# Kernel optimization log

Measured on AMD Instinct MI355X. Metric: run time of the kernel, lower is better.

## Reference

```python
import jax, jax.numpy as jnp
import numpy as np

D_MODEL = 1024
NHEAD = 16
HEAD_DIM = D_MODEL // NHEAD
B, S = 4, 2048


def setup_inputs() -> dict:
    key = jax.random.key(0)
    ks = jax.random.split(key, 10)
    scale = 1.0 / np.sqrt(D_MODEL)
    inp = {
        "x": jax.random.normal(ks[0], (B, S, D_MODEL), dtype=jnp.float32),
        "y": jax.random.normal(ks[1], (B, S, D_MODEL), dtype=jnp.float32),
        "wq": jax.random.normal(ks[2], (D_MODEL, D_MODEL), dtype=jnp.float32) * scale,
        "bq": jnp.zeros((D_MODEL,), dtype=jnp.float32),
        "wk": jax.random.normal(ks[3], (D_MODEL, D_MODEL), dtype=jnp.float32) * scale,
        "bk": jnp.zeros((D_MODEL,), dtype=jnp.float32),
        "wv": jax.random.normal(ks[4], (D_MODEL, D_MODEL), dtype=jnp.float32) * scale,
        "bv": jnp.zeros((D_MODEL,), dtype=jnp.float32),
        "wo": jax.random.normal(ks[5], (D_MODEL, D_MODEL), dtype=jnp.float32) * scale,
        "bo": jnp.zeros((D_MODEL,), dtype=jnp.float32),
    }
    return inp


def reference(x, y, wq, bq, wk, bk, wv, bv, wo, bo):
    # Linear projections (torch nn.Linear: x @ W.T + b; here weights stored as [in, out])
    q = x @ wq + bq  # [B, S, D]
    k = y @ wk + bk
    v = y @ wv + bv
    # split heads -> [B, H, S, Dh]
    def heads(t):
        return t.reshape(B, S, NHEAD, HEAD_DIM).transpose(0, 2, 1, 3)
    q, k, v = heads(q), heads(k), heads(v)
    scores = jnp.einsum("bhqd,bhkd->bhqk", q, k) / jnp.sqrt(jnp.float32(HEAD_DIM))
    attn = jax.nn.softmax(scores, axis=-1)  # dropout = identity in eval mode
    out = jnp.einsum("bhqk,bhkd->bhqd", attn, v)
    out = out.transpose(0, 2, 1, 3).reshape(B, S, D_MODEL)
    return out @ wo + bo
```

## Files before the change

### kernel.cpp

```cpp
#include <hip/hip_runtime.h>
#include <stdint.h>

#define D_MODEL 1024
#define NHEAD 16
#define HEAD_DIM 64
#define BATCH 4
#define SEQ 2048
#define ROWS (BATCH*SEQ)

typedef __attribute__((ext_vector_type(8))) short short8;
typedef __attribute__((ext_vector_type(4))) float f32x4;
typedef __attribute__((ext_vector_type(2))) unsigned int u32x2;
typedef unsigned short u16;
typedef unsigned int u32;

#define QSCALE 0.18033688011112042f

__device__ __forceinline__ u16 f2b(float f) {
  union { float f; uint32_t u; } in; in.f = f;
  uint32_t u = in.u;
  return (u16)((u + 0x7FFFu + ((u >> 16) & 1u)) >> 16);
}

__device__ __forceinline__ void async_lds16(const void* g, void* l) {
  __builtin_amdgcn_global_load_lds(
      (const __attribute__((address_space(1))) uint32_t*)g,
      (__attribute__((address_space(3))) uint32_t*)l,
      16, 0, 0);
}

__device__ __forceinline__ u32 pack_bf16(float lo, float hi) {
  union { float f; uint32_t u; } a, b; a.f = lo; b.f = hi;
  return __builtin_amdgcn_perm(b.u + 0x8000u, a.u + 0x8000u, 0x07060302u);
}

__global__ void __launch_bounds__(256) cvt_kernel(const float* __restrict__ in,
                                                  u16* __restrict__ out) {
  int i = blockIdx.x * 256 + threadIdx.x;
  float4 v = ((const float4*)in)[i];
  ushort4 o;
  o.x = f2b(v.x); o.y = f2b(v.y); o.z = f2b(v.z); o.w = f2b(v.w);
  ((ushort4*)out)[i] = o;
}

__global__ void __launch_bounds__(256) wtrans_kernel(const float* __restrict__ w,
                                                     u16* __restrict__ wt) {
  __shared__ u16 tile[64 * 65];
  int t = threadIdx.x;
  int c = t & 63, rb = t >> 6;
  int k0 = blockIdx.x * 64, n0 = blockIdx.y * 64;
#pragma unroll
  for (int i = 0; i < 16; ++i) {
    int r = rb + i * 4;
    tile[c * 65 + r] = f2b(w[(size_t)(k0 + r) * D_MODEL + n0 + c]);
  }
  __syncthreads();
#pragma unroll
  for (int i = 0; i < 16; ++i) {
    int r = rb + i * 4;
    wt[(size_t)(n0 + r) * D_MODEL + k0 + c] = tile[r * 65 + c];
  }
}

template <int MODE>
__device__ __forceinline__ void gemm_bt_core(const u16* __restrict__ A,
                                             const u16* __restrict__ Bt,
                                             const float* __restrict__ bias,
                                             void* __restrict__ Cout, float scale) {
  constexpr int K = 1024, N = 1024;
  __shared__ u16 As[128 * 32];
  __shared__ u16 Bs[128 * 32];
  int tid = threadIdx.x;
  int wave = tid >> 6, lane = tid & 63;
  int quad = lane >> 4, l16 = lane & 15;
  int wm = wave & 1, wn = wave >> 1;
  int m0 = blockIdx.y * 128, n0 = blockIdx.x * 128;

  f32x4 acc[4][4];
#pragma unroll
  for (int mi = 0; mi < 4; ++mi)
#pragma unroll
    for (int ni = 0; ni < 4; ++ni) acc[mi][ni] = f32x4{0.f, 0.f, 0.f, 0.f};

  int srow = lane >> 2;
  int scol = (lane & 3) * 16;

  for (int k0 = 0; k0 < K; k0 += 32) {
#pragma unroll
    for (int i = 0; i < 2; ++i) {
      int c = wave * 2 + i;
      const char* ga = (const char*)(A + (size_t)(m0 + c * 16 + srow) * K + k0) + scol;
      async_lds16(ga, (char*)As + c * 1024);
      const char* gb = (const char*)(Bt + (size_t)(n0 + c * 16 + srow) * K + k0) + scol;
      async_lds16(gb, (char*)Bs + c * 1024);
    }
    __syncthreads();

    short8 af[4], bf[4];
#pragma unroll
    for (int mi = 0; mi < 4; ++mi)
      af[mi] = *(const short8*)(As + (wm * 64 + mi * 16 + l16) * 32 + quad * 8);
#pragma unroll
    for (int ni = 0; ni < 4; ++ni)
      bf[ni] = *(const short8*)(Bs + (wn * 64 + ni * 16 + l16) * 32 + quad * 8);
#pragma unroll
    for (int mi = 0; mi < 4; ++mi)
#pragma unroll
      for (int ni = 0; ni < 4; ++ni)
        acc[mi][ni] = __builtin_amdgcn_mfma_f32_16x16x32_bf16(af[mi], bf[ni], acc[mi][ni], 0, 0, 0);
    __syncthreads();
  }

  if (MODE == 2) {
#pragma unroll
    for (int ni = 0; ni < 4; ++ni) {
      int col = n0 + wn * 64 + ni * 16 + l16;
      int bb = col >> 11, ss = col & 2047;
      size_t sbase = (size_t)(ss & ~63) + 4 * l16 + ni;
#pragma unroll
      for (int mi = 0; mi < 4; ++mi) {
        int row0 = m0 + wm * 64 + mi * 16 + quad * 4;
#pragma unroll
        for (int r = 0; r < 4; ++r) {
          int dcol = row0 + r;
          float vv = acc[mi][ni][r] + bias[dcol];
          int hh = dcol >> 6, dd = dcol & 63;
          size_t vtrow = ((size_t)bb * 16 + hh) * 64 + dd;
          ((u16*)Cout)[vtrow * 2048 + sbase] = f2b(vv);
        }
      }
    }
  } else {
#pragma unroll
    for (int ni = 0; ni < 4; ++ni) {
      int col = n0 + wn * 64 + ni * 16 + l16;
      float bv = bias[col];
#pragma unroll
      for (int mi = 0; mi < 4; ++mi) {
        int row = m0 + wm * 64 + mi * 16 + quad * 4;
#pragma unroll
        for (int r = 0; r < 4; ++r) {
          float vv = (acc[mi][ni][r] + bv) * scale;
          if (MODE == 1)
            ((float*)Cout)[(size_t)(row + r) * N + col] = vv;
          else
            ((u16*)Cout)[(size_t)(row + r) * N + col] = f2b(vv);
        }
      }
    }
  }
}

__global__ void __launch_bounds__(256) gemm_qk_kernel(
    const u16* __restrict__ xb, const u16* __restrict__ yb,
    const u16* __restrict__ wqT, const u16* __restrict__ wkT,
    const float* __restrict__ bq, const float* __restrict__ bk,
    u16* __restrict__ q, u16* __restrict__ k) {
  if (blockIdx.z == 0)
    gemm_bt_core<0>(xb, wqT, bq, q, QSCALE);
  else
    gemm_bt_core<0>(yb, wkT, bk, k, 1.0f);
}

__global__ void __launch_bounds__(256) gemm_v_kernel(const u16* __restrict__ wvT,
                                                     const u16* __restrict__ yb,
                                                     const float* __restrict__ bv,
                                                     u16* __restrict__ vt) {
  gemm_bt_core<2>(wvT, yb, bv, vt, 1.0f);
}

__global__ void __launch_bounds__(256) gemm_o_kernel(const u16* __restrict__ ao,
                                                     const u16* __restrict__ woT,
                                                     const float* __restrict__ bo,
                                                     float* __restrict__ out) {
  gemm_bt_core<1>(ao, woT, bo, out, 1.0f);
}

__global__ void __launch_bounds__(256, 4) attn_kernel(const u16* __restrict__ Q,
                                                      const u16* __restrict__ Kp,
                                                      const u16* __restrict__ Vt,
                                                      u16* __restrict__ Outp) {
  __shared__ u16 Ks[64 * 64];
  __shared__ u16 Vts[64 * 64];
  __shared__ u16 Ps[4][32 * 64];

  int tid = threadIdx.x, wave = tid >> 6, lane = tid & 63;
  int quad = lane >> 4, l16 = lane & 15;
  int bh = blockIdx.y;
  int b = bh >> 4, h = bh & 15;
  int q0 = blockIdx.x * 128 + wave * 32;
  size_t gbase = (size_t)b * SEQ * D_MODEL;
  const u16* kbase = Kp + gbase + (size_t)h * HEAD_DIM;
  const u16* vbase = Vt + (size_t)bh * HEAD_DIM * SEQ;
  const u16* qrow = Q + gbase + (size_t)q0 * D_MODEL + (size_t)h * HEAD_DIM;

  short8 aq[2][2];
#pragma unroll
  for (int rs = 0; rs < 2; ++rs)
#pragma unroll
    for (int dc = 0; dc < 2; ++dc)
      aq[rs][dc] = *(const short8*)(qrow + (size_t)(rs * 16 + l16) * D_MODEL + dc * 32 + quad * 8);

  f32x4 Oacc[2][4];
  float lpart[2][4];
#pragma unroll
  for (int rs = 0; rs < 2; ++rs)
#pragma unroll
    for (int ni = 0; ni < 4; ++ni) Oacc[rs][ni] = f32x4{0.f, 0.f, 0.f, 0.f};
#pragma unroll
  for (int rs = 0; rs < 2; ++rs)
#pragma unroll
    for (int r = 0; r < 4; ++r) lpart[rs][r] = 0.f;

  size_t koff[2], voff[2];
  int dstoff[2];
#pragma unroll
  for (int i = 0; i < 2; ++i) {
    int c = i * 256 + tid;
    int krow = c >> 3, kgp = c & 7;
    koff[i] = (size_t)krow * D_MODEL + (size_t)((kgp ^ (krow & 7)) * 8);
    voff[i] = (size_t)krow * SEQ + (size_t)((kgp ^ (krow & 7)) * 8);
    dstoff[i] = i * 4096 + wave * 1024;
  }

  for (int kv0 = 0; kv0 < SEQ; kv0 += 64) {
    __syncthreads();
#pragma unroll
    for (int i = 0; i < 2; ++i) {
      async_lds16(kbase + (size_t)kv0 * D_MODEL + koff[i], (char*)Ks + dstoff[i]);
      async_lds16(vbase + (size_t)kv0 + voff[i], (char*)Vts + dstoff[i]);
    }
    __syncthreads();

    u16* Pw = Ps[wave];
#pragma unroll
    for (int rs = 0; rs < 2; ++rs) {
      f32x4 S[4];
#pragma unroll
      for (int sub = 0; sub < 4; ++sub) {
        int key = sub * 16 + l16;
        int x = l16 & 7;
        short8 b0 = *(const short8*)(Ks + key * 64 + ((quad ^ x) << 3));
        short8 b1 = *(const short8*)(Ks + key * 64 + (((4 + quad) ^ x) << 3));
        f32x4 s = f32x4{0.f, 0.f, 0.f, 0.f};
        s = __builtin_amdgcn_mfma_f32_16x16x32_bf16(aq[rs][0], b0, s, 0, 0, 0);
        s = __builtin_amdgcn_mfma_f32_16x16x32_bf16(aq[rs][1], b1, s, 0, 0, 0);
        S[sub] = s;
      }
#pragma unroll
      for (int r = 0; r < 4; ++r) {
        float p0 = __builtin_amdgcn_exp2f(S[0][r]);
        float p1 = __builtin_amdgcn_exp2f(S[1][r]);
        float p2 = __builtin_amdgcn_exp2f(S[2][r]);
        float p3 = __builtin_amdgcn_exp2f(S[3][r]);
        lpart[rs][r] += (p0 + p1) + (p2 + p3);
        u32 lo = pack_bf16(p0, p1);
        u32 hi = pack_bf16(p2, p3);
        int row = rs * 16 + quad * 4 + r;
        int off = row * 64 + (((l16 >> 1) ^ (row & 7)) << 3) + ((l16 & 1) << 2);
        *(u32x2*)(Pw + off) = u32x2{lo, hi};
      }
    }

#pragma unroll
    for (int kc = 0; kc < 2; ++kc) {
      short8 pa[2];
#pragma unroll
      for (int rs = 0; rs < 2; ++rs) {
        int prow = rs * 16 + l16;
        pa[rs] = *(const short8*)(Pw + prow * 64 + ((((kc << 2) + quad) ^ (l16 & 7)) << 3));
      }
#pragma unroll
      for (int ni = 0; ni < 4; ++ni) {
        int d = ni * 16 + l16;
        short8 bv = *(const short8*)(Vts + d * 64 + ((((kc << 2) + quad) ^ (l16 & 7)) << 3));
        Oacc[0][ni] = __builtin_amdgcn_mfma_f32_16x16x32_bf16(pa[0], bv, Oacc[0][ni], 0, 0, 0);
        Oacc[1][ni] = __builtin_amdgcn_mfma_f32_16x16x32_bf16(pa[1], bv, Oacc[1][ni], 0, 0, 0);
      }
    }
  }

#pragma unroll
  for (int rs = 0; rs < 2; ++rs)
#pragma unroll
    for (int r = 0; r < 4; ++r) {
      float l = lpart[rs][r];
      l += __shfl_xor(l, 1);
      l += __shfl_xor(l, 2);
      l += __shfl_xor(l, 4);
      l += __shfl_xor(l, 8);
      float inv = 1.0f / l;
      size_t orow = gbase + (size_t)(q0 + rs * 16 + quad * 4 + r) * D_MODEL + (size_t)h * HEAD_DIM;
#pragma unroll
      for (int ni = 0; ni < 4; ++ni)
        Outp[orow + ni * 16 + l16] = f2b(Oacc[rs][ni][r] * inv);
    }
}

extern "C" void kernel_launch(void* const* d_in, const int* in_sizes, int n_in,
                              void* d_out, int out_size, void* d_ws, size_t ws_size,
                              hipStream_t stream) {
  const float* x  = (const float*)d_in[0];
  const float* y  = (const float*)d_in[1];
  const float* wq = (const float*)d_in[2];
  const float* bq = (const float*)d_in[3];
  const float* wk = (const float*)d_in[4];
  const float* bk = (const float*)d_in[5];
  const float* wv = (const float*)d_in[6];
  const float* bv = (const float*)d_in[7];
  const float* wo = (const float*)d_in[8];
  const float* bo = (const float*)d_in[9];
  float* out = (float*)d_out;

  char* ws = (char*)d_ws;
  const size_t SZ_ACT = (size_t)ROWS * D_MODEL * 2;
  const size_t SZ_W   = (size_t)D_MODEL * D_MODEL * 2;
  u16* xb  = (u16*)(ws);
  u16* yb  = (u16*)(ws + SZ_ACT);
  u16* wqT = (u16*)(ws + 2 * SZ_ACT);
  u16* wkT = (u16*)(ws + 2 * SZ_ACT + SZ_W);
  u16* wvT = (u16*)(ws + 2 * SZ_ACT + 2 * SZ_W);
  u16* woT = (u16*)(ws + 2 * SZ_ACT + 3 * SZ_W);
  u16* qb  = (u16*)(ws + 2 * SZ_ACT + 4 * SZ_W);
  u16* kb  = (u16*)(ws + 3 * SZ_ACT + 4 * SZ_W);
  u16* vt  = (u16*)(ws + 4 * SZ_ACT + 4 * SZ_W);
  u16* ao  = (u16*)(ws + 5 * SZ_ACT + 4 * SZ_W);

  cvt_kernel<<<8192, 256, 0, stream>>>(x, xb);
  cvt_kernel<<<8192, 256, 0, stream>>>(y, yb);
  wtrans_kernel<<<dim3(16, 16), 256, 0, stream>>>(wq, wqT);
  wtrans_kernel<<<dim3(16, 16), 256, 0, stream>>>(wk, wkT);
  wtrans_kernel<<<dim3(16, 16), 256, 0, stream>>>(wv, wvT);
  wtrans_kernel<<<dim3(16, 16), 256, 0, stream>>>(wo, woT);
  gemm_qk_kernel<<<dim3(8, 64, 2), 256, 0, stream>>>(xb, yb, wqT, wkT, bq, bk, qb, kb);
  gemm_v_kernel<<<dim3(64, 8), 256, 0, stream>>>(wvT, yb, bv, vt);
  attn_kernel<<<dim3(16, 64), 256, 0, stream>>>(qb, kb, vt, ao);
  gemm_o_kernel<<<dim3(8, 64), 256, 0, stream>>>(ao, woT, bo, out);
}
```

Baseline: 346.3 us.

## Double-buffer attention K/V tiles, merge launches, and reorder attention grid

```diff
diff --git a/kernel.cpp b/kernel.cpp
--- a/kernel.cpp
+++ b/kernel.cpp
@@ -34,8 +34,12 @@
   return __builtin_amdgcn_perm(b.u + 0x8000u, a.u + 0x8000u, 0x07060302u);
 }
 
-__global__ void __launch_bounds__(256) cvt_kernel(const float* __restrict__ in,
-                                                  u16* __restrict__ out) {
+__global__ void __launch_bounds__(256) cvt_kernel(const float* __restrict__ x,
+                                                  const float* __restrict__ y,
+                                                  u16* __restrict__ xb,
+                                                  u16* __restrict__ yb) {
+  const float* in = blockIdx.y ? y : x;
+  u16* out = blockIdx.y ? yb : xb;
   int i = blockIdx.x * 256 + threadIdx.x;
   float4 v = ((const float4*)in)[i];
   ushort4 o;
@@ -43,9 +47,15 @@
   ((ushort4*)out)[i] = o;
 }
 
-__global__ void __launch_bounds__(256) wtrans_kernel(const float* __restrict__ w,
-                                                     u16* __restrict__ wt) {
+__global__ void __launch_bounds__(256) wtrans_kernel(const float* __restrict__ wq,
+                                                     const float* __restrict__ wk,
+                                                     const float* __restrict__ wv,
+                                                     const float* __restrict__ wo,
+                                                     u16* __restrict__ wtbase) {
   __shared__ u16 tile[64 * 65];
+  int z = blockIdx.z;
+  const float* w = (z == 0) ? wq : (z == 1 ? wk : (z == 2 ? wv : wo));
+  u16* wt = wtbase + (size_t)z * D_MODEL * D_MODEL;
   int t = threadIdx.x;
   int c = t & 63, rb = t >> 6;
   int k0 = blockIdx.x * 64, n0 = blockIdx.y * 64;
@@ -66,7 +76,8 @@
 __device__ __forceinline__ void gemm_bt_core(const u16* __restrict__ A,
                                              const u16* __restrict__ Bt,
                                              const float* __restrict__ bias,
-                                             void* __restrict__ Cout, float scale) {
+                                             void* __restrict__ Cout, float scale,
+                                             int m0, int n0) {
   constexpr int K = 1024, N = 1024;
   __shared__ u16 As[128 * 32];
   __shared__ u16 Bs[128 * 32];
@@ -74,7 +85,6 @@
   int wave = tid >> 6, lane = tid & 63;
   int quad = lane >> 4, l16 = lane & 15;
   int wm = wave & 1, wn = wave >> 1;
-  int m0 = blockIdx.y * 128, n0 = blockIdx.x * 128;
 
   f32x4 acc[4][4];
 #pragma unroll
@@ -151,44 +161,41 @@
   }
 }
 
-__global__ void __launch_bounds__(256) gemm_qk_kernel(
+__global__ void __launch_bounds__(256) gemm_qkv_kernel(
     const u16* __restrict__ xb, const u16* __restrict__ yb,
-    const u16* __restrict__ wqT, const u16* __restrict__ wkT,
-    const float* __restrict__ bq, const float* __restrict__ bk,
-    u16* __restrict__ q, u16* __restrict__ k) {
-  if (blockIdx.z == 0)
-    gemm_bt_core<0>(xb, wqT, bq, q, QSCALE);
-  else
-    gemm_bt_core<0>(yb, wkT, bk, k, 1.0f);
-}
-
-__global__ void __launch_bounds__(256) gemm_v_kernel(const u16* __restrict__ wvT,
-                                                     const u16* __restrict__ yb,
-                                                     const float* __restrict__ bv,
-                                                     u16* __restrict__ vt) {
-  gemm_bt_core<2>(wvT, yb, bv, vt, 1.0f);
+    const u16* __restrict__ wqT, const u16* __restrict__ wkT, const u16* __restrict__ wvT,
+    const float* __restrict__ bq, const float* __restrict__ bk, const float* __restrict__ bv,
+    u16* __restrict__ q, u16* __restrict__ k, u16* __restrict__ vt) {
+  int bx = blockIdx.x, z = blockIdx.y;
+  if (z == 0) {
+    gemm_bt_core<0>(xb, wqT, bq, q, QSCALE, (bx >> 3) * 128, (bx & 7) * 128);
+  } else if (z == 1) {
+    gemm_bt_core<0>(yb, wkT, bk, k, 1.0f, (bx >> 3) * 128, (bx & 7) * 128);
+  } else {
+    gemm_bt_core<2>(wvT, yb, bv, vt, 1.0f, (bx & 7) * 128, (bx >> 3) * 128);
+  }
 }
 
 __global__ void __launch_bounds__(256) gemm_o_kernel(const u16* __restrict__ ao,
                                                      const u16* __restrict__ woT,
                                                      const float* __restrict__ bo,
                                                      float* __restrict__ out) {
-  gemm_bt_core<1>(ao, woT, bo, out, 1.0f);
+  gemm_bt_core<1>(ao, woT, bo, out, 1.0f, blockIdx.y * 128, blockIdx.x * 128);
 }
 
 __global__ void __launch_bounds__(256, 4) attn_kernel(const u16* __restrict__ Q,
                                                       const u16* __restrict__ Kp,
                                                       const u16* __restrict__ Vt,
                                                       u16* __restrict__ Outp) {
-  __shared__ u16 Ks[64 * 64];
-  __shared__ u16 Vts[64 * 64];
+  __shared__ u16 Ks[2][64 * 64];
+  __shared__ u16 Vts[2][64 * 64];
   __shared__ u16 Ps[4][32 * 64];
 
   int tid = threadIdx.x, wave = tid >> 6, lane = tid & 63;
   int quad = lane >> 4, l16 = lane & 15;
-  int bh = blockIdx.y;
+  int bh = blockIdx.x;
   int b = bh >> 4, h = bh & 15;
-  int q0 = blockIdx.x * 128 + wave * 32;
+  int q0 = blockIdx.y * 128 + wave * 32;
   size_t gbase = (size_t)b * SEQ * D_MODEL;
   const u16* kbase = Kp + gbase + (size_t)h * HEAD_DIM;
   const u16* vbase = Vt + (size_t)bh * HEAD_DIM * SEQ;
@@ -223,28 +230,46 @@
     dstoff[i] = i * 4096 + wave * 1024;
   }
 
-  for (int kv0 = 0; kv0 < SEQ; kv0 += 64) {
+#pragma unroll
+  for (int i = 0; i < 2; ++i) {
+    async_lds16(kbase + koff[i], (char*)Ks[0] + dstoff[i]);
+    async_lds16(vbase + voff[i], (char*)Vts[0] + dstoff[i]);
+  }
+
+  constexpr int NT = SEQ / 64;
+  for (int t = 0; t < NT; ++t) {
+    int cur = t & 1;
     __syncthreads();
-#pragma unroll
-    for (int i = 0; i < 2; ++i) {
-      async_lds16(kbase + (size_t)kv0 * D_MODEL + koff[i], (char*)Ks + dstoff[i]);
-      async_lds16(vbase + (size_t)kv0 + voff[i], (char*)Vts + dstoff[i]);
-    }
-    __syncthreads();
-
+    if (t + 1 < NT) {
+      size_t kvoff = (size_t)(t + 1) * 64;
+#pragma unroll
+      for (int i = 0; i < 2; ++i) {
+        async_lds16(kbase + kvoff * D_MODEL + koff[i], (char*)Ks[cur ^ 1] + dstoff[i]);
+        async_lds16(vbase + kvoff + voff[i], (char*)Vts[cur ^ 1] + dstoff[i]);
+      }
+    }
+
+    const u16* Kc = Ks[cur];
+    const u16* Vc = Vts[cur];
     u16* Pw = Ps[wave];
+    int x = l16 & 7;
+
+    short8 kf[4][2];
+#pragma unroll
+    for (int sub = 0; sub < 4; ++sub) {
+      const u16* kr = Kc + (sub * 16 + l16) * 64;
+      kf[sub][0] = *(const short8*)(kr + ((quad ^ x) << 3));
+      kf[sub][1] = *(const short8*)(kr + (((4 + quad) ^ x) << 3));
+    }
+
 #pragma unroll
     for (int rs = 0; rs < 2; ++rs) {
       f32x4 S[4];
 #pragma unroll
       for (int sub = 0; sub < 4; ++sub) {
-        int key = sub * 16 + l16;
-        int x = l16 & 7;
-        short8 b0 = *(const short8*)(Ks + key * 64 + ((quad ^ x) << 3));
-        short8 b1 = *(const short8*)(Ks + key * 64 + (((4 + quad) ^ x) << 3));
         f32x4 s = f32x4{0.f, 0.f, 0.f, 0.f};
-        s = __builtin_amdgcn_mfma_f32_16x16x32_bf16(aq[rs][0], b0, s, 0, 0, 0);
-        s = __builtin_amdgcn_mfma_f32_16x16x32_bf16(aq[rs][1], b1, s, 0, 0, 0);
+        s = __builtin_amdgcn_mfma_f32_16x16x32_bf16(aq[rs][0], kf[sub][0], s, 0, 0, 0);
+        s = __builtin_amdgcn_mfma_f32_16x16x32_bf16(aq[rs][1], kf[sub][1], s, 0, 0, 0);
         S[sub] = s;
       }
 #pragma unroll
@@ -268,12 +293,12 @@
 #pragma unroll
       for (int rs = 0; rs < 2; ++rs) {
         int prow = rs * 16 + l16;
-        pa[rs] = *(const short8*)(Pw + prow * 64 + ((((kc << 2) + quad) ^ (l16 & 7)) << 3));
+        pa[rs] = *(const short8*)(Pw + prow * 64 + ((((kc << 2) + quad) ^ x) << 3));
       }
 #pragma unroll
       for (int ni = 0; ni < 4; ++ni) {
         int d = ni * 16 + l16;
-        short8 bv = *(const short8*)(Vts + d * 64 + ((((kc << 2) + quad) ^ (l16 & 7)) << 3));
+        short8 bv = *(const short8*)(Vc + d * 64 + ((((kc << 2) + quad) ^ (l16 & 7)) << 3));
         Oacc[0][ni] = __builtin_amdgcn_mfma_f32_16x16x32_bf16(pa[0], bv, Oacc[0][ni], 0, 0, 0);
         Oacc[1][ni] = __builtin_amdgcn_mfma_f32_16x16x32_bf16(pa[1], bv, Oacc[1][ni], 0, 0, 0);
       }
@@ -317,7 +342,8 @@
   const size_t SZ_W   = (size_t)D_MODEL * D_MODEL * 2;
   u16* xb  = (u16*)(ws);
   u16* yb  = (u16*)(ws + SZ_ACT);
-  u16* wqT = (u16*)(ws + 2 * SZ_ACT);
+  u16* wT  = (u16*)(ws + 2 * SZ_ACT);
+  u16* wqT = wT;
   u16* wkT = (u16*)(ws + 2 * SZ_ACT + SZ_W);
   u16* wvT = (u16*)(ws + 2 * SZ_ACT + 2 * SZ_W);
   u16* woT = (u16*)(ws + 2 * SZ_ACT + 3 * SZ_W);
@@ -326,14 +352,9 @@
   u16* vt  = (u16*)(ws + 4 * SZ_ACT + 4 * SZ_W);
   u16* ao  = (u16*)(ws + 5 * SZ_ACT + 4 * SZ_W);
 
-  cvt_kernel<<<8192, 256, 0, stream>>>(x, xb);
-  cvt_kernel<<<8192, 256, 0, stream>>>(y, yb);
-  wtrans_kernel<<<dim3(16, 16), 256, 0, stream>>>(wq, wqT);
-  wtrans_kernel<<<dim3(16, 16), 256, 0, stream>>>(wk, wkT);
-  wtrans_kernel<<<dim3(16, 16), 256, 0, stream>>>(wv, wvT);
-  wtrans_kernel<<<dim3(16, 16), 256, 0, stream>>>(wo, woT);
-  gemm_qk_kernel<<<dim3(8, 64, 2), 256, 0, stream>>>(xb, yb, wqT, wkT, bq, bk, qb, kb);
-  gemm_v_kernel<<<dim3(64, 8), 256, 0, stream>>>(wvT, yb, bv, vt);
-  attn_kernel<<<dim3(16, 64), 256, 0, stream>>>(qb, kb, vt, ao);
+  cvt_kernel<<<dim3(8192, 2), 256, 0, stream>>>(x, y, xb, yb);
+  wtrans_kernel<<<dim3(16, 16, 4), 256, 0, stream>>>(wq, wk, wv, wo, wT);
+  gemm_qkv_kernel<<<dim3(512, 3), 256, 0, stream>>>(xb, yb, wqT, wkT, wvT, bq, bk, bv, qb, kb, vt);
+  attn_kernel<<<dim3(64, 16), 256, 0, stream>>>(qb, kb, vt, ao);
   gemm_o_kernel<<<dim3(8, 64), 256, 0, stream>>>(ao, woT, bo, out);
 }
```

Result: no change. 352.2 us (+1.7%).
